# Kernel tuning notes

Measured on AMD Instinct MI355X. Metric: run time of the kernel, lower is better.

The kernel has to match this reference:

```python
import jax, jax.numpy as jnp
import numpy as np

N = 1024
IN_F = 256
OUT_F = 128
H = 4
NH = OUT_F // H  # 32
NEG_SLOPE = 0.2


def setup_inputs() -> dict:
    key = jax.random.key(0)
    k1, k2, k3, k4, k5 = jax.random.split(key, 5)
    h = jax.random.normal(k1, (N, IN_F), dtype=jnp.float32)
    adj_mat = jax.random.randint(k2, (N, N, 1), 0, 2, dtype=jnp.int32)
    s_in = 1.0 / np.sqrt(IN_F)
    s_nh = 1.0 / np.sqrt(NH)
    Wl = jax.random.uniform(k3, (H * NH, IN_F), jnp.float32, -s_in, s_in)
    Wr = jax.random.uniform(k4, (H * NH, IN_F), jnp.float32, -s_in, s_in)
    attn_w = jax.random.uniform(k5, (NH,), jnp.float32, -s_nh, s_nh)
    return {"h": h, "adj_mat": adj_mat, "Wl": Wl, "Wr": Wr, "attn_w": attn_w}


def reference(h, adj_mat, Wl, Wr, attn_w):
    n = h.shape[0]
    g_l = (h @ Wl.T).reshape(n, H, NH)  # [N,H,F]
    g_r = (h @ Wr.T).reshape(n, H, NH)  # [N,H,F]
    # g_sum[i, j] = g_l[j] + g_r[i]  (repeat / repeat_interleave semantics)
    g_sum = g_l[None, :, :, :] + g_r[:, None, :, :]  # [N,N,H,F]
    act = jnp.where(g_sum >= 0, g_sum, NEG_SLOPE * g_sum)
    e = jnp.einsum('ijhf,f->ijh', act, attn_w)  # [N,N,H]
    mask = adj_mat != 0  # [N,N,1] broadcasts over heads
    e = jnp.where(mask, e, -jnp.inf)
    a = jax.nn.softmax(e, axis=1)  # softmax over source nodes j
    h_prime = jnp.einsum('ijh,jhf->ihf', a, g_r).reshape(n, H * NH)
    # is_output_layer=False -> ELU (dropout is a no-op in eval)
    return jax.nn.elu(h_prime)
```

## Files before the change

kernel.cpp:

```cpp
#include <hip/hip_runtime.h>
#include <math.h>

typedef float v2f __attribute__((ext_vector_type(2)));

#define NN 1024
#define IN_F 256
#define OUT_F 128
#define NHEADS 4
#define NHF 32

__global__ void __launch_bounds__(256) glr_gemm(const float* __restrict__ hmat,
                                                const float* __restrict__ Wl,
                                                const float* __restrict__ Wr,
                                                v2f* __restrict__ glT,
                                                float* __restrict__ grh) {
    __shared__ float hs[64 * 132];
    const int tid  = threadIdx.x;
    const int rg   = blockIdx.x;
    const int cs   = blockIdx.y;
    const int lane = tid & 63;
    const int wu   = __builtin_amdgcn_readfirstlane(tid >> 6);
    const int c0   = cs * 8 + wu * 2;
    const int half = c0 >> 7;
    const int cc   = c0 & 127;
    const float* __restrict__ W   = half ? Wr : Wl;
    const float* __restrict__ wr0 = W + cc * IN_F;
    const float* __restrict__ wr1 = wr0 + IN_F;

    float a0 = 0.f, a1 = 0.f;
    for (int kh = 0; kh < 2; ++kh) {
#pragma unroll
        for (int s = 0; s < 8; ++s) {
            const int v = tid + s * 256;
            const int row = v >> 5, q = v & 31;
            const float4 x = ((const float4*)hmat)[(rg * 64 + row) * 64 + kh * 32 + q];
            *(float4*)(hs + row * 132 + q * 4) = x;
        }
        __syncthreads();
        const float4* __restrict__ w0p = (const float4*)(wr0 + kh * 128);
        const float4* __restrict__ w1p = (const float4*)(wr1 + kh * 128);
        const float*  __restrict__ hrow = hs + lane * 132;
#pragma unroll 8
        for (int q = 0; q < 32; ++q) {
            const float4 hv = *(const float4*)(hrow + q * 4);
            const float4 w0 = w0p[q];
            const float4 w1 = w1p[q];
            a0 = fmaf(hv.x, w0.x, fmaf(hv.y, w0.y, fmaf(hv.z, w0.z, fmaf(hv.w, w0.w, a0))));
            a1 = fmaf(hv.x, w1.x, fmaf(hv.y, w1.y, fmaf(hv.z, w1.z, fmaf(hv.w, w1.w, a1))));
        }
        __syncthreads();
    }

    const int row = rg * 64 + lane;
    const int hh = cc >> 5, f0 = cc & 31;
    if (half == 0) {
        glT[(hh * 16 + (f0 >> 1)) * NN + row] = (v2f){a0, a1};
    } else {
        *(v2f*)(grh + (hh * NN + row) * NHF + f0) = (v2f){a0, a1};
    }
}

__global__ void __launch_bounds__(512, 4) gat_main(const v2f* __restrict__ glT,
                                                   const float* __restrict__ grh,
                                                   const int* __restrict__ adj,
                                                   const float* __restrict__ attn_w,
                                                   float* __restrict__ out) {
    const int hh   = blockIdx.y;
    const int i0   = blockIdx.x * 8;
    const int tid  = threadIdx.x;
    const int lane = tid & 63;
    const int wv   = __builtin_amdgcn_readfirstlane(tid >> 6);

    __shared__ float p_buf[8][NN];
    __shared__ float alpha_s[NN];
    __shared__ float g_t[128 * 33];
    __shared__ float l_sh[8];

    const v2f* __restrict__ w2p    = (const v2f*)attn_w;
    const v2f* __restrict__ glbase = glT + hh * 16 * NN;

#pragma unroll
    for (int c = 0; c < 2; ++c) {
        const int j = (c << 9) + tid;
        const v2f* __restrict__ glp = glbase + j;
        v2f aa = {0.f, 0.f};
#pragma unroll
        for (int fp = 0; fp < 16; ++fp) aa += glp[fp * NN] * w2p[fp];
        alpha_s[j] = 0.6f * (aa.x + aa.y);
    }

    const v2f* __restrict__ gr2 = (const v2f*)(grh + (hh * NN + i0 + wv) * NHF);
    v2f grr[16];
#pragma unroll
    for (int fp = 0; fp < 16; ++fp) grr[fp] = gr2[fp];

    __syncthreads();

    const int* __restrict__ adjrow = adj + (i0 + wv) * NN;
    float lsum = 0.f;
    for (int t = 0; t < 16; ++t) {
        const int j = (t << 6) + lane;
        const v2f* __restrict__ glp = glbase + j;
        v2f gl2[16];
#pragma unroll
        for (int fp = 0; fp < 16; ++fp) gl2[fp] = glp[fp * NN];
        const int ad = adjrow[j];
        v2f S = {0.f, 0.f};
#pragma unroll
        for (int fp = 0; fp < 16; ++fp) {
            const v2f s = gl2[fp] + grr[fp];
            const v2f m = __builtin_elementwise_max(s, -s);
            S += m * w2p[fp];
        }
        const float e = fmaf(0.4f, S.x + S.y, alpha_s[j]);
        const float p = ad ? __expf(e) : 0.f;
        p_buf[wv][j] = p;
        lsum += p;
    }
#pragma unroll
    for (int d = 32; d > 0; d >>= 1) lsum += __shfl_xor(lsum, d);
    if (lane == 0) l_sh[wv] = lsum;

    v2f acc[8][2];
#pragma unroll
    for (int ii = 0; ii < 8; ++ii) { acc[ii][0] = (v2f){0.f, 0.f}; acc[ii][1] = (v2f){0.f, 0.f}; }

    const float4* __restrict__ gsrc = (const float4*)(grh + hh * NN * NHF);
    for (int t = 0; t < 8; ++t) {
        __syncthreads();
#pragma unroll
        for (int s2 = 0; s2 < 2; ++s2) {
            const int u = tid + (s2 << 9);
            const int jj = u >> 3, f4 = u & 7;
            const float4 x = gsrc[(t << 10) + u];
            *(float4*)&g_t[jj * 33 + (f4 << 2)] = x;
        }
        __syncthreads();
#pragma unroll
        for (int u2 = 0; u2 < 2; ++u2) {
            const int jl = lane + (u2 << 6);
            const float4 g = *(const float4*)&g_t[jl * 33 + (wv << 2)];
            const int jg = (t << 7) + jl;
            float pv[8];
#pragma unroll
            for (int ii = 0; ii < 8; ++ii) pv[ii] = p_buf[ii][jg];
            const v2f g01 = {g.x, g.y}, g23 = {g.z, g.w};
#pragma unroll
            for (int ii = 0; ii < 8; ++ii) {
                const v2f pp = {pv[ii], pv[ii]};
                acc[ii][0] += pp * g01;
                acc[ii][1] += pp * g23;
            }
        }
    }

    float o32[32];
#pragma unroll
    for (int ii = 0; ii < 8; ++ii) {
        o32[ii * 4 + 0] = acc[ii][0].x;  o32[ii * 4 + 1] = acc[ii][0].y;
        o32[ii * 4 + 2] = acc[ii][1].x;  o32[ii * 4 + 3] = acc[ii][1].y;
    }
#pragma unroll
    for (int d = 32; d > 0; d >>= 1) {
#pragma unroll
        for (int k = 0; k < 32; ++k) o32[k] += __shfl_xor(o32[k], d);
    }
    if (lane == 0) {
#pragma unroll
        for (int ii = 0; ii < 8; ++ii) {
            const float inv = 1.f / l_sh[ii];
            const float x0 = o32[ii * 4 + 0] * inv;
            const float x1 = o32[ii * 4 + 1] * inv;
            const float x2 = o32[ii * 4 + 2] * inv;
            const float x3 = o32[ii * 4 + 3] * inv;
            float4 r;
            r.x = (x0 > 0.f) ? x0 : (__expf(x0) - 1.f);
            r.y = (x1 > 0.f) ? x1 : (__expf(x1) - 1.f);
            r.z = (x2 > 0.f) ? x2 : (__expf(x2) - 1.f);
            r.w = (x3 > 0.f) ? x3 : (__expf(x3) - 1.f);
            *(float4*)(out + (i0 + ii) * OUT_F + hh * NHF + (wv << 2)) = r;
        }
    }
}

extern "C" void kernel_launch(void* const* d_in, const int* in_sizes, int n_in,
                              void* d_out, int out_size, void* d_ws, size_t ws_size,
                              hipStream_t stream) {
    const float* hmat = (const float*)d_in[0];
    const int*   adj  = (const int*)d_in[1];
    const float* Wl   = (const float*)d_in[2];
    const float* Wr   = (const float*)d_in[3];
    const float* aw   = (const float*)d_in[4];
    float* o          = (float*)d_out;

    float* wsf = (float*)d_ws;
    v2f*   glT = (v2f*)wsf;
    float* grh = wsf + NHEADS * 16 * NN * 2;

    glr_gemm<<<dim3(16, 32), dim3(256), 0, stream>>>(hmat, Wl, Wr, glT, grh);
    gat_main<<<dim3(NN / 8, NHEADS), dim3(512), 0, stream>>>(glT, grh, adj, aw, o);
}
```

Baseline: 118.3 us.

## Process 16 target rows per block with j-parallel scoring and transposed g_r

Each block now handles 16 target rows instead of 8. Threads are assigned over source nodes j, so each g_l column is loaded once and reused across 16 rows, with the 16 g_r rows staged in shared memory. The GEMM kernel also writes a transposed copy of g_r, so the aggregation phase reads it with coalesced global loads instead of staging tiles through LDS. Row sums are folded into the final shuffle reduction. In exchange, register pressure rises (launch bounds drop to 2 blocks), there are half as many blocks (256), and the 80-value shuffle reduction costs more.

```diff
diff --git a/kernel.cpp b/kernel.cpp
--- a/kernel.cpp
+++ b/kernel.cpp
@@ -13,7 +13,8 @@
                                                 const float* __restrict__ Wl,
                                                 const float* __restrict__ Wr,
                                                 v2f* __restrict__ glT,
-                                                float* __restrict__ grh) {
+                                                float* __restrict__ grh,
+                                                v2f* __restrict__ grT) {
     __shared__ float hs[64 * 132];
     const int tid  = threadIdx.x;
     const int rg   = blockIdx.x;
@@ -57,122 +58,109 @@
         glT[(hh * 16 + (f0 >> 1)) * NN + row] = (v2f){a0, a1};
     } else {
         *(v2f*)(grh + (hh * NN + row) * NHF + f0) = (v2f){a0, a1};
+        grT[(hh * 16 + (f0 >> 1)) * NN + row] = (v2f){a0, a1};
     }
 }
 
-__global__ void __launch_bounds__(512, 4) gat_main(const v2f* __restrict__ glT,
+__global__ void __launch_bounds__(512, 2) gat_main(const v2f* __restrict__ glT,
                                                    const float* __restrict__ grh,
+                                                   const v2f* __restrict__ grT,
                                                    const int* __restrict__ adj,
                                                    const float* __restrict__ attn_w,
                                                    float* __restrict__ out) {
     const int hh   = blockIdx.y;
-    const int i0   = blockIdx.x * 8;
+    const int i0   = blockIdx.x * 16;
     const int tid  = threadIdx.x;
     const int lane = tid & 63;
     const int wv   = __builtin_amdgcn_readfirstlane(tid >> 6);
 
-    __shared__ float p_buf[8][NN];
-    __shared__ float alpha_s[NN];
-    __shared__ float g_t[128 * 33];
-    __shared__ float l_sh[8];
+    __shared__ float p_buf[16][NN];
+    __shared__ float grt[16][NHF];
+
+    if (tid < 16 * NHF) ((float*)grt)[tid] = grh[(hh * NN + i0) * NHF + tid];
 
     const v2f* __restrict__ w2p    = (const v2f*)attn_w;
     const v2f* __restrict__ glbase = glT + hh * 16 * NN;
+    __syncthreads();
 
-#pragma unroll
     for (int c = 0; c < 2; ++c) {
         const int j = (c << 9) + tid;
-        const v2f* __restrict__ glp = glbase + j;
-        v2f aa = {0.f, 0.f};
-#pragma unroll
-        for (int fp = 0; fp < 16; ++fp) aa += glp[fp * NN] * w2p[fp];
-        alpha_s[j] = 0.6f * (aa.x + aa.y);
-    }
-
-    const v2f* __restrict__ gr2 = (const v2f*)(grh + (hh * NN + i0 + wv) * NHF);
-    v2f grr[16];
-#pragma unroll
-    for (int fp = 0; fp < 16; ++fp) grr[fp] = gr2[fp];
-
-    __syncthreads();
-
-    const int* __restrict__ adjrow = adj + (i0 + wv) * NN;
-    float lsum = 0.f;
-    for (int t = 0; t < 16; ++t) {
-        const int j = (t << 6) + lane;
         const v2f* __restrict__ glp = glbase + j;
         v2f gl2[16];
 #pragma unroll
         for (int fp = 0; fp < 16; ++fp) gl2[fp] = glp[fp * NN];
-        const int ad = adjrow[j];
-        v2f S = {0.f, 0.f};
+
+        v2f aa = {0.f, 0.f};
 #pragma unroll
-        for (int fp = 0; fp < 16; ++fp) {
-            const v2f s = gl2[fp] + grr[fp];
-            const v2f m = __builtin_elementwise_max(s, -s);
-            S += m * w2p[fp];
+        for (int fp = 0; fp < 16; ++fp) aa += gl2[fp] * w2p[fp];
+        const float alpha6 = 0.6f * (aa.x + aa.y);
+
+        int adjv[16];
+#pragma unroll
+        for (int ii = 0; ii < 16; ++ii) adjv[ii] = adj[(i0 + ii) * NN + j];
+
+#pragma unroll
+        for (int ii = 0; ii < 16; ++ii) {
+            const v2f* __restrict__ grp = (const v2f*)grt[ii];
+            v2f S = {0.f, 0.f};
+#pragma unroll
+            for (int fp = 0; fp < 16; ++fp) {
+                const v2f s = gl2[fp] + grp[fp];
+                const v2f m = __builtin_elementwise_max(s, -s);
+                S += m * w2p[fp];
+            }
+            const float e = fmaf(0.4f, S.x + S.y, alpha6);
+            p_buf[ii][j] = adjv[ii] ? __expf(e) : 0.f;
         }
-        const float e = fmaf(0.4f, S.x + S.y, alpha_s[j]);
-        const float p = ad ? __expf(e) : 0.f;
-        p_buf[wv][j] = p;
-        lsum += p;
     }
+    __syncthreads();
+
+    const v2f* __restrict__ g0p = grT + (hh * 16 + wv * 2 + 0) * NN;
+    const v2f* __restrict__ g1p = grT + (hh * 16 + wv * 2 + 1) * NN;
+    v2f acc[16][2];
+    float lsum[16];
 #pragma unroll
-    for (int d = 32; d > 0; d >>= 1) lsum += __shfl_xor(lsum, d);
-    if (lane == 0) l_sh[wv] = lsum;
-
-    v2f acc[8][2];
+    for (int ii = 0; ii < 16; ++ii) {
+        acc[ii][0] = (v2f){0.f, 0.f};
+        acc[ii][1] = (v2f){0.f, 0.f};
+        lsum[ii] = 0.f;
+    }
+    for (int g = 0; g < 16; ++g) {
+        const int jq = (g << 6) + lane;
+        const v2f g01 = g0p[jq];
+        const v2f g23 = g1p[jq];
+        float pv[16];
 #pragma unroll
-    for (int ii = 0; ii < 8; ++ii) { acc[ii][0] = (v2f){0.f, 0.f}; acc[ii][1] = (v2f){0.f, 0.f}; }
-
-    const float4* __restrict__ gsrc = (const float4*)(grh + hh * NN * NHF);
-    for (int t = 0; t < 8; ++t) {
-        __syncthreads();
+        for (int ii = 0; ii < 16; ++ii) pv[ii] = p_buf[ii][jq];
 #pragma unroll
-        for (int s2 = 0; s2 < 2; ++s2) {
-            const int u = tid + (s2 << 9);
-            const int jj = u >> 3, f4 = u & 7;
-            const float4 x = gsrc[(t << 10) + u];
-            *(float4*)&g_t[jj * 33 + (f4 << 2)] = x;
-        }
-        __syncthreads();
-#pragma unroll
-        for (int u2 = 0; u2 < 2; ++u2) {
-            const int jl = lane + (u2 << 6);
-            const float4 g = *(const float4*)&g_t[jl * 33 + (wv << 2)];
-            const int jg = (t << 7) + jl;
-            float pv[8];
-#pragma unroll
-            for (int ii = 0; ii < 8; ++ii) pv[ii] = p_buf[ii][jg];
-            const v2f g01 = {g.x, g.y}, g23 = {g.z, g.w};
-#pragma unroll
-            for (int ii = 0; ii < 8; ++ii) {
-                const v2f pp = {pv[ii], pv[ii]};
-                acc[ii][0] += pp * g01;
-                acc[ii][1] += pp * g23;
-            }
+        for (int ii = 0; ii < 16; ++ii) {
+            const v2f pp = {pv[ii], pv[ii]};
+            acc[ii][0] += pp * g01;
+            acc[ii][1] += pp * g23;
+            lsum[ii] += pv[ii];
         }
     }
 
-    float o32[32];
+    float rv[80];
 #pragma unroll
-    for (int ii = 0; ii < 8; ++ii) {
-        o32[ii * 4 + 0] = acc[ii][0].x;  o32[ii * 4 + 1] = acc[ii][0].y;
-        o32[ii * 4 + 2] = acc[ii][1].x;  o32[ii * 4 + 3] = acc[ii][1].y;
+    for (int ii = 0; ii < 16; ++ii) {
+        rv[ii * 4 + 0] = acc[ii][0].x;  rv[ii * 4 + 1] = acc[ii][0].y;
+        rv[ii * 4 + 2] = acc[ii][1].x;  rv[ii * 4 + 3] = acc[ii][1].y;
+        rv[64 + ii] = lsum[ii];
     }
 #pragma unroll
     for (int d = 32; d > 0; d >>= 1) {
 #pragma unroll
-        for (int k = 0; k < 32; ++k) o32[k] += __shfl_xor(o32[k], d);
+        for (int k = 0; k < 80; ++k) rv[k] += __shfl_xor(rv[k], d);
     }
     if (lane == 0) {
 #pragma unroll
-        for (int ii = 0; ii < 8; ++ii) {
-            const float inv = 1.f / l_sh[ii];
-            const float x0 = o32[ii * 4 + 0] * inv;
-            const float x1 = o32[ii * 4 + 1] * inv;
-            const float x2 = o32[ii * 4 + 2] * inv;
-            const float x3 = o32[ii * 4 + 3] * inv;
+        for (int ii = 0; ii < 16; ++ii) {
+            const float inv = 1.f / rv[64 + ii];
+            const float x0 = rv[ii * 4 + 0] * inv;
+            const float x1 = rv[ii * 4 + 1] * inv;
+            const float x2 = rv[ii * 4 + 2] * inv;
+            const float x3 = rv[ii * 4 + 3] * inv;
             float4 r;
             r.x = (x0 > 0.f) ? x0 : (__expf(x0) - 1.f);
             r.y = (x1 > 0.f) ? x1 : (__expf(x1) - 1.f);
@@ -196,7 +184,8 @@
     float* wsf = (float*)d_ws;
     v2f*   glT = (v2f*)wsf;
     float* grh = wsf + NHEADS * 16 * NN * 2;
+    v2f*   grT = (v2f*)(grh + NHEADS * NN * NHF);
 
-    glr_gemm<<<dim3(16, 32), dim3(256), 0, stream>>>(hmat, Wl, Wr, glT, grh);
-    gat_main<<<dim3(NN / 8, NHEADS), dim3(512), 0, stream>>>(glT, grh, adj, aw, o);
+    glr_gemm<<<dim3(16, 32), dim3(256), 0, stream>>>(hmat, Wl, Wr, glT, grh, grT);
+    gat_main<<<dim3(NN / 16, NHEADS), dim3(512), 0, stream>>>(glT, grh, grT, adj, aw, o);
 }
```

Result: slower. 170.3 us (+43.9%).

## Use chunked gl/gr layouts, 1024-thread blocks, and drop LDS staging of g_r

Applied to the files above, without the earlier changes.

The GEMM kernel now writes g_l and an extra copy of g_r in a chunked [head][64-row chunk][feature pair][lane] layout. The main kernel doubles its block to 1024 threads, so each row's source range is split across two wave halves. The aggregation phase reads g_r straight from global memory in the new layout, replacing the shared-memory tile and its per-tile barriers. Partial row sums and outputs are combined through small shared buffers before the ELU, at the cost of extra workspace writes and a final cross-wave reduction.

```diff
diff --git a/kernel.cpp b/kernel.cpp
--- a/kernel.cpp
+++ b/kernel.cpp
@@ -12,8 +12,9 @@
 __global__ void __launch_bounds__(256) glr_gemm(const float* __restrict__ hmat,
                                                 const float* __restrict__ Wl,
                                                 const float* __restrict__ Wr,
-                                                v2f* __restrict__ glT,
-                                                float* __restrict__ grh) {
+                                                v2f* __restrict__ glC,
+                                                float* __restrict__ grh,
+                                                v2f* __restrict__ grC) {
     __shared__ float hs[64 * 132];
     const int tid  = threadIdx.x;
     const int rg   = blockIdx.x;
@@ -52,59 +53,64 @@
     }
 
     const int row = rg * 64 + lane;
-    const int hh = cc >> 5, f0 = cc & 31;
+    const int hh = cc >> 5, fp = (cc & 31) >> 1;
     if (half == 0) {
-        glT[(hh * 16 + (f0 >> 1)) * NN + row] = (v2f){a0, a1};
+        glC[((hh * 16 + rg) * 16 + fp) * 64 + lane] = (v2f){a0, a1};
     } else {
-        *(v2f*)(grh + (hh * NN + row) * NHF + f0) = (v2f){a0, a1};
+        *(v2f*)(grh + (hh * NN + row) * NHF + (cc & 31)) = (v2f){a0, a1};
+        grC[((hh * 16 + rg) * 16 + fp) * 64 + lane] = (v2f){a0, a1};
     }
 }
 
-__global__ void __launch_bounds__(512, 4) gat_main(const v2f* __restrict__ glT,
-                                                   const float* __restrict__ grh,
-                                                   const int* __restrict__ adj,
-                                                   const float* __restrict__ attn_w,
-                                                   float* __restrict__ out) {
+__global__ void __launch_bounds__(1024, 8) gat_main(const v2f* __restrict__ glC,
+                                                    const float* __restrict__ grh,
+                                                    const v2f* __restrict__ grC,
+                                                    const int* __restrict__ adj,
+                                                    const float* __restrict__ attn_w,
+                                                    float* __restrict__ out) {
     const int hh   = blockIdx.y;
     const int i0   = blockIdx.x * 8;
     const int tid  = threadIdx.x;
     const int lane = tid & 63;
     const int wv   = __builtin_amdgcn_readfirstlane(tid >> 6);
+    const int ii   = wv & 7;
+    const int hf   = wv >> 3;
 
     __shared__ float p_buf[8][NN];
     __shared__ float alpha_s[NN];
-    __shared__ float g_t[128 * 33];
+    __shared__ float lpart[8][2];
     __shared__ float l_sh[8];
-
-    const v2f* __restrict__ w2p    = (const v2f*)attn_w;
-    const v2f* __restrict__ glbase = glT + hh * 16 * NN;
-
-#pragma unroll
-    for (int c = 0; c < 2; ++c) {
-        const int j = (c << 9) + tid;
-        const v2f* __restrict__ glp = glbase + j;
+    __shared__ float opart[2][8][8][4];
+
+    const v2f* __restrict__ w2p = (const v2f*)attn_w;
+
+    {
+        const int ch = tid >> 6;
+        const v2f* __restrict__ gp = glC + ((hh * 16 + ch) * 16) * 64 + (tid & 63);
         v2f aa = {0.f, 0.f};
 #pragma unroll
-        for (int fp = 0; fp < 16; ++fp) aa += glp[fp * NN] * w2p[fp];
-        alpha_s[j] = 0.6f * (aa.x + aa.y);
-    }
-
-    const v2f* __restrict__ gr2 = (const v2f*)(grh + (hh * NN + i0 + wv) * NHF);
+        for (int fp = 0; fp < 16; ++fp) aa += gp[fp * 64] * w2p[fp];
+        alpha_s[tid] = 0.6f * (aa.x + aa.y);
+    }
+
+    const v2f* __restrict__ gr2 = (const v2f*)(grh + (hh * NN + i0 + ii) * NHF);
     v2f grr[16];
 #pragma unroll
     for (int fp = 0; fp < 16; ++fp) grr[fp] = gr2[fp];
 
     __syncthreads();
 
-    const int* __restrict__ adjrow = adj + (i0 + wv) * NN;
+    const int* __restrict__ adjrow = adj + (i0 + ii) * NN + (hf << 9);
+    float* __restrict__ prow = &p_buf[ii][hf << 9];
+    const float* __restrict__ arow = &alpha_s[hf << 9];
     float lsum = 0.f;
-    for (int t = 0; t < 16; ++t) {
-        const int j = (t << 6) + lane;
-        const v2f* __restrict__ glp = glbase + j;
+    for (int g = 0; g < 8; ++g) {
+        const int jl = (g << 6) + lane;
+        const v2f* __restrict__ gp = glC + ((hh * 16 + (hf << 3) + g) * 16) * 64 + lane;
         v2f gl2[16];
 #pragma unroll
-        for (int fp = 0; fp < 16; ++fp) gl2[fp] = glp[fp * NN];
-        const int ad = adjrow[j];
+        for (int fp = 0; fp < 16; ++fp) gl2[fp] = gp[fp * 64];
+        const int ad = adjrow[jl];
         v2f S = {0.f, 0.f};
 #pragma unroll
         for (int fp = 0; fp < 16; ++fp) {
@@ -112,74 +118,66 @@
             const v2f m = __builtin_elementwise_max(s, -s);
             S += m * w2p[fp];
         }
-        const float e = fmaf(0.4f, S.x + S.y, alpha_s[j]);
+        const float e = fmaf(0.4f, S.x + S.y, arow[jl]);
         const float p = ad ? __expf(e) : 0.f;
-        p_buf[wv][j] = p;
+        prow[jl] = p;
         lsum += p;
     }
 #pragma unroll
     for (int d = 32; d > 0; d >>= 1) lsum += __shfl_xor(lsum, d);
-    if (lane == 0) l_sh[wv] = lsum;
+    if (lane == 0) lpart[ii][hf] = lsum;
+    __syncthreads();
+    if (tid < 8) l_sh[tid] = lpart[tid][0] + lpart[tid][1];
 
     v2f acc[8][2];
 #pragma unroll
-    for (int ii = 0; ii < 8; ++ii) { acc[ii][0] = (v2f){0.f, 0.f}; acc[ii][1] = (v2f){0.f, 0.f}; }
-
-    const float4* __restrict__ gsrc = (const float4*)(grh + hh * NN * NHF);
-    for (int t = 0; t < 8; ++t) {
-        __syncthreads();
-#pragma unroll
-        for (int s2 = 0; s2 < 2; ++s2) {
-            const int u = tid + (s2 << 9);
-            const int jj = u >> 3, f4 = u & 7;
-            const float4 x = gsrc[(t << 10) + u];
-            *(float4*)&g_t[jj * 33 + (f4 << 2)] = x;
-        }
-        __syncthreads();
-#pragma unroll
-        for (int u2 = 0; u2 < 2; ++u2) {
-            const int jl = lane + (u2 << 6);
-            const float4 g = *(const float4*)&g_t[jl * 33 + (wv << 2)];
-            const int jg = (t << 7) + jl;
-            float pv[8];
-#pragma unroll
-            for (int ii = 0; ii < 8; ++ii) pv[ii] = p_buf[ii][jg];
-            const v2f g01 = {g.x, g.y}, g23 = {g.z, g.w};
-#pragma unroll
-            for (int ii = 0; ii < 8; ++ii) {
-                const v2f pp = {pv[ii], pv[ii]};
-                acc[ii][0] += pp * g01;
-                acc[ii][1] += pp * g23;
-            }
-        }
-    }
-
-    float o32[32];
-#pragma unroll
-    for (int ii = 0; ii < 8; ++ii) {
-        o32[ii * 4 + 0] = acc[ii][0].x;  o32[ii * 4 + 1] = acc[ii][0].y;
-        o32[ii * 4 + 2] = acc[ii][1].x;  o32[ii * 4 + 3] = acc[ii][1].y;
+    for (int k = 0; k < 8; ++k) { acc[k][0] = (v2f){0.f, 0.f}; acc[k][1] = (v2f){0.f, 0.f}; }
+    const int q = ii;
+    for (int g = 0; g < 8; ++g) {
+        const int ch = (hf << 3) + g;
+        const v2f* __restrict__ gp = grC + ((hh * 16 + ch) * 16) * 64 + lane;
+        const v2f g01 = gp[(2 * q) * 64];
+        const v2f g23 = gp[(2 * q + 1) * 64];
+        const float* __restrict__ pb = &p_buf[0][(ch << 6) + lane];
+        float pv[8];
+#pragma unroll
+        for (int k = 0; k < 8; ++k) pv[k] = pb[k * NN];
+#pragma unroll
+        for (int k = 0; k < 8; ++k) {
+            const v2f pp = {pv[k], pv[k]};
+            acc[k][0] += pp * g01;
+            acc[k][1] += pp * g23;
+        }
+    }
+
+    float rv[32];
+#pragma unroll
+    for (int k = 0; k < 8; ++k) {
+        rv[k * 4 + 0] = acc[k][0].x;  rv[k * 4 + 1] = acc[k][0].y;
+        rv[k * 4 + 2] = acc[k][1].x;  rv[k * 4 + 3] = acc[k][1].y;
     }
 #pragma unroll
     for (int d = 32; d > 0; d >>= 1) {
 #pragma unroll
-        for (int k = 0; k < 32; ++k) o32[k] += __shfl_xor(o32[k], d);
+        for (int k = 0; k < 32; ++k) rv[k] += __shfl_xor(rv[k], d);
     }
     if (lane == 0) {
 #pragma unroll
-        for (int ii = 0; ii < 8; ++ii) {
-            const float inv = 1.f / l_sh[ii];
-            const float x0 = o32[ii * 4 + 0] * inv;
-            const float x1 = o32[ii * 4 + 1] * inv;
-            const float x2 = o32[ii * 4 + 2] * inv;
-            const float x3 = o32[ii * 4 + 3] * inv;
-            float4 r;
-            r.x = (x0 > 0.f) ? x0 : (__expf(x0) - 1.f);
-            r.y = (x1 > 0.f) ? x1 : (__expf(x1) - 1.f);
-            r.z = (x2 > 0.f) ? x2 : (__expf(x2) - 1.f);
-            r.w = (x3 > 0.f) ? x3 : (__expf(x3) - 1.f);
-            *(float4*)(out + (i0 + ii) * OUT_F + hh * NHF + (wv << 2)) = r;
-        }
+        for (int k = 0; k < 8; ++k) {
+            opart[hf][q][k][0] = rv[k * 4 + 0];
+            opart[hf][q][k][1] = rv[k * 4 + 1];
+            opart[hf][q][k][2] = rv[k * 4 + 2];
+            opart[hf][q][k][3] = rv[k * 4 + 3];
+        }
+    }
+    __syncthreads();
+
+    if (tid < 256) {
+        const int io = tid >> 5, ff = tid & 31;
+        const float o = (opart[0][ff >> 2][io][ff & 3] + opart[1][ff >> 2][io][ff & 3])
+                        / l_sh[io];
+        const float r = (o > 0.f) ? o : (__expf(o) - 1.f);
+        out[(i0 + io) * OUT_F + hh * NHF + ff] = r;
     }
 }
 
@@ -194,9 +192,10 @@
     float* o          = (float*)d_out;
 
     float* wsf = (float*)d_ws;
-    v2f*   glT = (v2f*)wsf;
-    float* grh = wsf + NHEADS * 16 * NN * 2;
-
-    glr_gemm<<<dim3(16, 32), dim3(256), 0, stream>>>(hmat, Wl, Wr, glT, grh);
-    gat_main<<<dim3(NN / 8, NHEADS), dim3(512), 0, stream>>>(glT, grh, adj, aw, o);
+    v2f*   glC = (v2f*)wsf;
+    float* grh = wsf + 131072;
+    v2f*   grC = (v2f*)(wsf + 262144);
+
+    glr_gemm<<<dim3(16, 32), dim3(256), 0, stream>>>(hmat, Wl, Wr, glC, grh, grC);
+    gat_main<<<dim3(NN / 8, NHEADS), dim3(1024), 0, stream>>>(glC, grh, grC, adj, aw, o);
 }
```

Result: slower. 130.1 us (+9.9%).
